# Kernel optimization log

Measured on AMD Instinct MI355X. Metric: run time of the kernel, lower is better.

## Reference

```python
import jax, jax.numpy as jnp
import numpy as np

EPS = 1e-5
K = 20  # n. neighbors


def _lrelu(x):
    return jnp.where(x >= 0, x, 0.2 * x)


def _bn(x, gamma, beta):
    # training-mode batchnorm over all axes except channel axis 1
    axes = tuple(i for i in range(x.ndim) if i != 1)
    m = jnp.mean(x, axis=axes, keepdims=True)
    v = jnp.var(x, axis=axes, keepdims=True)
    shape = [1, x.shape[1]] + [1] * (x.ndim - 2)
    return (x - m) * jax.lax.rsqrt(v + EPS) * gamma.reshape(shape) + beta.reshape(shape)


def _knn(x, k):
    # x: (B, C, N) -> idx (B, N, k) of nearest neighbors (largest negative sq dist)
    xx = jnp.sum(x * x, axis=1)                      # (B, N)
    inner = jnp.einsum('bcn,bcm->bnm', x, x)          # (B, N, N)
    dist = -xx[:, :, None] + 2.0 * inner - xx[:, None, :]
    _, idx = jax.lax.top_k(dist, k)
    return idx


def _graph_feature(x, k):
    # x: (B, C, N) -> edge features (B, 2C, N, k)
    B = x.shape[0]
    idx = _knn(x, k)                                  # (B, N, k)
    xt = jnp.transpose(x, (0, 2, 1))                  # (B, N, C)
    nbr = xt[jnp.arange(B)[:, None, None], idx]       # (B, N, k, C)
    ctr = xt[:, :, None, :]                           # (B, N, 1, C)
    edge = jnp.concatenate([nbr - ctr, jnp.broadcast_to(ctr, nbr.shape)], axis=-1)
    return jnp.transpose(edge, (0, 3, 1, 2))          # (B, 2C, N, k)


def _conv1d(W, x):
    return jnp.einsum('oc,bcn->bon', W, x)


def _conv2d(W, x):
    return jnp.einsum('oc,bcnk->bonk', W, x)


def setup_inputs() -> dict:
    key = jax.random.key(0)
    ks = jax.random.split(key, 10)
    w = lambda k, s: jax.random.normal(k, s, jnp.float32) * 0.05
    d = {
        'x': jax.random.normal(ks[0], (4, 3, 4096), jnp.float32),
        'W1': w(ks[1], (64, 3)),
        'W2': w(ks[2], (64, 128)),
        'W3': w(ks[3], (64, 128)),
        'W4': w(ks[4], (512, 64)),
        'W5': w(ks[5], (512, 704)),
        'W6': w(ks[6], (256, 512)),
        'W7': w(ks[7], (128, 256)),
        'W8': w(ks[8], (2, 128)),
        'bias8': jnp.zeros((2,), jnp.float32),
    }
    bn_ch = [64, 64, 64, 512, 512, 256, 128]
    for i, c in enumerate(bn_ch, start=1):
        d[f'gamma{i}'] = jnp.ones((c,), jnp.float32)
        d[f'beta{i}'] = jnp.zeros((c,), jnp.float32)
    return d


def reference(x, W1, W2, W3, W4, W5, W6, W7, W8, bias8,
              gamma1, beta1, gamma2, beta2, gamma3, beta3, gamma4, beta4,
              gamma5, beta5, gamma6, beta6, gamma7, beta7):
    N = x.shape[2]
    x1 = _lrelu(_bn(_conv1d(W1, x), gamma1, beta1))                 # (B,64,N)
    e2 = _graph_feature(x1, K)                                      # (B,128,N,k)
    x2 = _lrelu(_bn(_conv2d(W2, e2), gamma2, beta2)).max(axis=-1)   # (B,64,N)
    e3 = _graph_feature(x2, K)
    x3 = _lrelu(_bn(_conv2d(W3, e3), gamma3, beta3)).max(axis=-1)   # (B,64,N)
    x6 = _lrelu(_bn(_conv1d(W4, x3), gamma4, beta4))                # (B,512,N)
    x6 = jnp.broadcast_to(x6.max(axis=-1, keepdims=True), (x6.shape[0], x6.shape[1], N))
    x7 = jnp.concatenate([x1, x2, x3, x6], axis=1)                  # (B,704,N)
    x7 = _lrelu(_bn(_conv1d(W5, x7), gamma5, beta5))
    x7 = _lrelu(_bn(_conv1d(W6, x7), gamma6, beta6))
    x7 = _lrelu(_bn(_conv1d(W7, x7), gamma7, beta7))
    return _conv1d(W8, x7) + bias8[None, :, None]                   # (B,2,N)
```

## Files before the change

kernel.cpp:

```cpp
#include <hip/hip_runtime.h>
#include <math.h>

#define NN 4096
#define BB 4
#define NPT (NN*BB)
#define KK 20
#define EPSB 1e-5f

#define AS_STRIDE 132
#define WS_STRIDE 68
#define SKEW(c) ((((((c)>>2)&7))<<2) + (((c)>>5)*28))

__device__ __forceinline__ float lrelu(float x){ return x >= 0.f ? x : 0.2f*x; }

__global__ void conv1_kernel(const float* __restrict__ x, const float* __restrict__ W1,
                             float* __restrict__ xcat){
  __shared__ float Wl[192];
  int tid = threadIdx.x;
  if (tid < 192) Wl[tid] = W1[tid];
  __syncthreads();
  int p = blockIdx.x*4 + (tid >> 6);
  int o = tid & 63;
  int b = p >> 12, n = p & 4095;
  const float* xb = x + (size_t)b*3*NN + n;
  float acc = Wl[o*3+0]*xb[0] + Wl[o*3+1]*xb[NN] + Wl[o*3+2]*xb[2*NN];
  xcat[(size_t)p*192 + o] = acc;
}

__global__ void stats_pm_kernel(const float* __restrict__ buf, int stride, int ofs,
                                float* __restrict__ psum, float* __restrict__ psumsq, int C){
  int tid = threadIdx.x;
  int lane = tid & 63, g = tid >> 6;
  int o = blockIdx.x*64 + lane;
  int p0 = blockIdx.y*256 + g*64;
  float s = 0.f, ss = 0.f;
  for (int i = 0; i < 64; ++i){
    float v = buf[(size_t)(p0+i)*stride + ofs + o];
    s += v; ss += v*v;
  }
  __shared__ float rs[4][64], rss[4][64];
  rs[g][lane] = s; rss[g][lane] = ss;
  __syncthreads();
  if (g == 0){
    s  = rs[0][lane]+rs[1][lane]+rs[2][lane]+rs[3][lane];
    ss = rss[0][lane]+rss[1][lane]+rss[2][lane]+rss[3][lane];
    psum[(size_t)blockIdx.y*C + o] = s;
// ... 12 lines not shown
  for (int i = 0; i < nparts; ++i){
    s  += psum[(size_t)i*C + o];
    ss += psumsq[(size_t)i*C + o];
  }
  float m = s*invcnt;
  float v = ss*invcnt - m*m;
  v = fmaxf(v, 0.f);
  float sc = gamma[o] * rsqrtf(v + EPSB);
  scale[o] = sc;
  shift[o] = beta[o] - m*sc;
}

__global__ void apply_bn_kernel(float* __restrict__ buf, int stride, int ofs, int log2C,
                                const float* __restrict__ scale, const float* __restrict__ shift){
  int i = blockIdx.x*256 + threadIdx.x;
  int o = i & ((1<<log2C)-1);
  int p = i >> log2C;
  size_t a = (size_t)p*stride + ofs + o;
  float e = buf[a]*scale[o] + shift[o];
  buf[a] = lrelu(e);
}

__global__ void xx_kernel(const float* __restrict__ xcat, int stride, int ofs,
                          float* __restrict__ xx){
  int p = blockIdx.x*256 + threadIdx.x;
  const float4* r = (const float4*)(xcat + (size_t)p*stride + ofs);
  float s = 0.f;
  #pragma unroll
  for (int i = 0; i < 16; ++i){ float4 v = r[i]; s += v.x*v.x + v.y*v.y + v.z*v.z + v.w*v.w; }
  xx[p] = s;
}

__global__ void __launch_bounds__(256, 2)
dist_kernel(const float* __restrict__ xcat, int ofs,
            const float* __restrict__ xx, float* __restrict__ dist, int b){
  __shared__ float As[64*AS_STRIDE + 64];
  __shared__ float Bs[64*AS_STRIDE + 64];
  int tid = threadIdx.x;
  int n0 = blockIdx.x*128, m0 = blockIdx.y*128;
  const float* base = xcat + (size_t)b*NN*192 + ofs;
  #pragma unroll
  for (int j = 0; j < 8; ++j){
    int slot = tid + 256*j;
    int row = slot >> 4, c4 = (slot & 15)*4;
    float4 v = *(const float4*)(base + (size_t)(n0+row)*192 + c4);
    As[(c4+0)*AS_STRIDE+SKEW(c4+0)+row]=v.x; As[(c4+1)*AS_STRIDE+SKEW(c4+1)+row]=v.y;
    As[(c4+2)*AS_STRIDE+SKEW(c4+2)+row]=v.z; As[(c4+3)*AS_STRIDE+SKEW(c4+3)+row]=v.w;
    float4 w = *(const float4*)(base + (size_t)(m0+row)*192 + c4);
    Bs[(c4+0)*AS_STRIDE+SKEW(c4+0)+row]=w.x; Bs[(c4+1)*AS_STRIDE+SKEW(c4+1)+row]=w.y;
    Bs[(c4+2)*AS_STRIDE+SKEW(c4+2)+row]=w.z; Bs[(c4+3)*AS_STRIDE+SKEW(c4+3)+row]=w.w;
  }
  __syncthreads();
  int pA = (tid >> 4)*4, oB = (tid & 15)*4;
  float acc[8][8] = {};
  for (int c = 0; c < 64; ++c){
    const float* arow = &As[c*AS_STRIDE + SKEW(c)];
    const float* brow = &Bs[c*AS_STRIDE + SKEW(c)];
    float4 a0 = *(const float4*)&arow[pA];
    float4 a1 = *(const float4*)&arow[pA + 64];
    float4 b0 = *(const float4*)&brow[oB];
    float4 b1 = *(const float4*)&brow[oB + 64];
    float av[8] = {a0.x,a0.y,a0.z,a0.w,a1.x,a1.y,a1.z,a1.w};
    float bv[8] = {b0.x,b0.y,b0.z,b0.w,b1.x,b1.y,b1.z,b1.w};
    #pragma unroll
    for (int i = 0; i < 8; ++i)
      #pragma unroll
      for (int j = 0; j < 8; ++j)
        acc[i][j] += av[i]*bv[j];
  }
  float xm[8];
  #pragma unroll
  for (int j = 0; j < 4; ++j){
    xm[j]   = xx[b*NN + m0 + oB + j];
    xm[4+j] = xx[b*NN + m0 + 64 + oB + j];
  }
  #pragma unroll
  for (int h = 0; h < 2; ++h){
    #pragma unroll
    for (int i = 0; i < 4; ++i){
      int row = n0 + h*64 + pA + i;
      float xn = xx[b*NN + row];
      int ai = h*4 + i;
      float4 w0, w1;
      w0.x = 2.f*acc[ai][0] - xn - xm[0]; w0.y = 2.f*acc[ai][1] - xn - xm[1];
      w0.z = 2.f*acc[ai][2] - xn - xm[2]; w0.w = 2.f*acc[ai][3] - xn - xm[3];
      w1.x = 2.f*acc[ai][4] - xn - xm[4]; w1.y = 2.f*acc[ai][5] - xn - xm[5];
      w1.z = 2.f*acc[ai][6] - xn - xm[6]; w1.w = 2.f*acc[ai][7] - xn - xm[7];
      float* drow = dist + (size_t)row*NN + m0;
      *(float4*)(drow + oB) = w0;
      *(float4*)(drow + 64 + oB) = w1;
    }
  }
}

__global__ void topk_kernel(const float* __restrict__ dist, int* __restrict__ idxout){
  int n = blockIdx.x;
  int tid = threadIdx.x;
  int wv = tid >> 6;
  const float* row = dist + (size_t)n*NN;
  unsigned k[16];
  #pragma unroll
  for (int i = 0; i < 16; ++i){
    unsigned u = __float_as_uint(row[tid + (i<<8)]);
    k[i] = u ^ (unsigned)(((int)u >> 31) | 0x80000000);
  }
  __shared__ unsigned hist[4][256];
  __shared__ unsigned sufx[257];
  __shared__ unsigned selw[1];
  __shared__ unsigned toff[256];
  __shared__ int mred[4];
  unsigned remaining = KK;
  unsigned prefix = 0;
  #pragma unroll
  for (int lvl = 0; lvl < 4; ++lvl){
    int shift = 24 - lvl*8;
    hist[0][tid]=0; hist[1][tid]=0; hist[2][tid]=0; hist[3][tid]=0;
    __syncthreads();
    unsigned pmask = (lvl == 0) ? 0u : (0xFFFFFFFFu << (shift + 8));
    #pragma unroll
    for (int i = 0; i < 16; ++i){
      if ((k[i] & pmask) == prefix)
        atomicAdd(&hist[wv][(k[i] >> shift) & 255], 1u);
    }
    __syncthreads();
    if (tid < 64){
      unsigned h[4];
      #pragma unroll
      for (int q = 0; q < 4; ++q)
        h[q] = hist[0][tid*4+q]+hist[1][tid*4+q]+hist[2][tid*4+q]+hist[3][tid*4+q];
      unsigned lane_sum = h[0]+h[1]+h[2]+h[3];
      unsigned acc = lane_sum;
      #pragma unroll
      for (int s = 1; s < 64; s <<= 1){
        unsigned o = __shfl_down(acc, s);
        if (tid + s < 64) acc += o;
      }
      unsigned excl = acc - lane_sum;
      sufx[tid*4+3] = excl + h[3];
      sufx[tid*4+2] = excl + h[3] + h[2];
      sufx[tid*4+1] = excl + h[3] + h[2] + h[1];
      sufx[tid*4+0] = excl + h[3] + h[2] + h[1] + h[0];
      if (tid == 0) sufx[256] = 0;
    }
    __syncthreads();
    unsigned s_d = sufx[tid], s_d1 = sufx[tid+1];
    if (s_d >= remaining && s_d1 < remaining) selw[0] = tid;
    __syncthreads();
    unsigned d = selw[0];
    remaining -= sufx[d+1];
    prefix |= d << shift;
  }
  unsigned K20 = prefix;
  unsigned r = remaining;
  unsigned mycount = 0;
  #pragma unroll
  for (int i = 0; i < 16; ++i) if (k[i] > K20) mycount++;
  toff[tid] = mycount;
  __syncthreads();
  if (tid < 64){
    unsigned c0=toff[tid*4], c1=toff[tid*4+1], c2=toff[tid*4+2], c3=toff[tid*4+3];
    unsigned lane_sum = c0+c1+c2+c3;
    unsigned acc = lane_sum;
    #pragma unroll
    for (int s = 1; s < 64; s <<= 1){
      unsigned o = __shfl_up(acc, s);
      if ((int)tid - s >= 0) acc += o;
    }
    unsigned excl = acc - lane_sum;
    sufx[tid*4+0] = excl;
    sufx[tid*4+1] = excl + c0;
    sufx[tid*4+2] = excl + c0 + c1;
    sufx[tid*4+3] = excl + c0 + c1 + c2;
  }
  __syncthreads();
  unsigned pos = sufx[tid];
  int* orow = idxout + n*KK;
  #pragma unroll
  for (int i = 0; i < 16; ++i)
    if (k[i] > K20) orow[pos++] = tid + (i<<8);
  unsigned A = KK - r;
  int last = -1;
  for (unsigned t = 0; t < r; ++t){
    int best = 0x7fffffff;
    #pragma unroll
    for (int i = 0; i < 16; ++i){
      int m = tid + (i<<8);
      if (k[i] == K20 && m > last && m < best) best = m;
    }
    #pragma unroll
    for (int s = 32; s > 0; s >>= 1){
      int o = __shfl_down(best, s);
      best = min(best, o);
    }
    if ((tid & 63) == 0) mred[tid >> 6] = best;
    __syncthreads();
    int w = min(min(mred[0],mred[1]), min(mred[2],mred[3]));
    if (tid == 0) orow[A + t] = w;
    last = w;
    __syncthreads();
  }
}

__global__ void ut_kernel(const float* __restrict__ xcat, int ofs, const float* __restrict__ W,
                          float* __restrict__ U, float* __restrict__ T){
  __shared__ float Wl[64*129];
  int tid = threadIdx.x;
  for (int i = tid; i < 64*128; i += 256){
    int o = i >> 7, c = i & 127;
    Wl[o*129 + c] = W[i];
  }
  __syncthreads();
  int g = tid >> 6, lane = tid & 63;
  int p = blockIdx.x*4 + g;
  float xv = xcat[(size_t)p*192 + ofs + lane];
  const float* wr = Wl + lane*129;
  float u = 0.f, t = 0.f;
  for (int c = 0; c < 64; ++c){
    float xc = __shfl(xv, c);
    float wa = wr[c], wb = wr[64+c];
    u += wa*xc;
    t += (wb - wa)*xc;
  }
  U[(size_t)p*64 + lane] = u;
  T[(size_t)p*64 + lane] = t;
}

__global__ void gather_kernel(const float* __restrict__ U, const float* __restrict__ T,
                              const int* __restrict__ idx,
                              float* __restrict__ psum, float* __restrict__ psumsq,
                              float* __restrict__ vmax, float* __restrict__ vmin){
  int tid = threadIdx.x;
  int g = tid >> 6, lane = tid & 63;
  int p0 = blockIdx.x*64 + g*16;
// ... 23 lines not shown
    psumsq[(size_t)blockIdx.x*64 + lane] = ss;
  }
}

__global__ void gapply_kernel(const float* __restrict__ vmax, const float* __restrict__ vmin,
                              const float* __restrict__ scale, const float* __restrict__ shift,
                              float* __restrict__ xcat, int ofs){
  int i = blockIdx.x*256 + threadIdx.x;
  int p = i >> 6, o = i & 63;
  float s = scale[o];
  float v = (s >= 0.f) ? vmax[i] : vmin[i];
  xcat[(size_t)p*192 + ofs + o] = lrelu(s*v + shift[o]);
}

__global__ void __launch_bounds__(256, 2)
mm_kernel(const float* __restrict__ in, int inStride, int inOfs,
          const float* __restrict__ W, int wStride,
          float* __restrict__ out, int outStride,
          const float* __restrict__ bias, int O, int I,
          const float* __restrict__ bnScale, const float* __restrict__ bnShift){
  __shared__ float As[64*AS_STRIDE + 64];
  __shared__ float Ws[64*WS_STRIDE + 64];
  int tid = threadIdx.x;
  int p0 = blockIdx.x*128, o0 = blockIdx.y*64;
  int psub = (tid >> 4)*8, osub = (tid & 15)*4;
  int cgrp = (tid & 15)*4;
  float acc[8][4] = {};
  for (int cc = 0; cc < I; cc += 64){
    float4 sc4 = make_float4(1.f,1.f,1.f,1.f), sh4 = make_float4(0.f,0.f,0.f,0.f);
    if (bnScale){
      sc4 = *(const float4*)(bnScale + cc + cgrp);
      sh4 = *(const float4*)(bnShift + cc + cgrp);
    }
    #pragma unroll
    for (int j = 0; j < 8; ++j){
      int slot = tid + 256*j;
      int row = slot >> 4, c4 = cgrp;
      float4 v = *(const float4*)(in + (size_t)(p0+row)*inStride + inOfs + cc + c4);
      if (bnScale){
        v.x = lrelu(v.x*sc4.x + sh4.x); v.y = lrelu(v.y*sc4.y + sh4.y);
        v.z = lrelu(v.z*sc4.z + sh4.z); v.w = lrelu(v.w*sc4.w + sh4.w);
      }
      As[(c4+0)*AS_STRIDE+SKEW(c4+0)+row]=v.x; As[(c4+1)*AS_STRIDE+SKEW(c4+1)+row]=v.y;
      As[(c4+2)*AS_STRIDE+SKEW(c4+2)+row]=v.z; As[(c4+3)*AS_STRIDE+SKEW(c4+3)+row]=v.w;
    }
    #pragma unroll
    for (int j = 0; j < 4; ++j){
      int slot = tid + 256*j;
      int row = slot >> 4, c4 = cgrp;
      float4 v = *(const float4*)(W + (size_t)(o0+row)*wStride + cc + c4);
      Ws[(c4+0)*WS_STRIDE+SKEW(c4+0)+row]=v.x; Ws[(c4+1)*WS_STRIDE+SKEW(c4+1)+row]=v.y;
      Ws[(c4+2)*WS_STRIDE+SKEW(c4+2)+row]=v.z; Ws[(c4+3)*WS_STRIDE+SKEW(c4+3)+row]=v.w;
    }
    __syncthreads();
    for (int c = 0; c < 64; ++c){
      const float* arow = &As[c*AS_STRIDE + SKEW(c)];
      const float* brow = &Ws[c*WS_STRIDE + SKEW(c)];
      float4 a0 = *(const float4*)&arow[psub];
      float4 a1 = *(const float4*)&arow[psub + 4];
      float4 bb = *(const float4*)&brow[osub];
      float av[8] = {a0.x,a0.y,a0.z,a0.w,a1.x,a1.y,a1.z,a1.w};
      float bv[4] = {bb.x,bb.y,bb.z,bb.w};
      #pragma unroll
      for (int i = 0; i < 8; ++i)
        #pragma unroll
        for (int j = 0; j < 4; ++j)
          acc[i][j] += av[i]*bv[j];
    }
    __syncthreads();
  }
  int bIdx = p0 >> 12;
  float bb0=0.f, bb1=0.f, bb2=0.f, bb3=0.f;
  if (bias){
    bb0 = bias[bIdx*O + o0 + osub + 0];
    bb1 = bias[bIdx*O + o0 + osub + 1];
    bb2 = bias[bIdx*O + o0 + osub + 2];
    bb3 = bias[bIdx*O + o0 + osub + 3];
  }
  #pragma unroll
  for (int i = 0; i < 8; ++i){
    float4 w;
    w.x = acc[i][0]+bb0; w.y = acc[i][1]+bb1; w.z = acc[i][2]+bb2; w.w = acc[i][3]+bb3;
    *(float4*)(out + (size_t)(p0+psub+i)*outStride + o0 + osub) = w;
  }
}

__global__ void __launch_bounds__(256, 2)
mm128_kernel(const float* __restrict__ in, int inStride, int inOfs,
             const float* __restrict__ W, int wStride,
             float* __restrict__ out, int outStride,
             const float* __restrict__ bias, int O, int I,
             const float* __restrict__ bnScale, const float* __restrict__ bnShift){
  __shared__ float As[64*AS_STRIDE + 64];
  __shared__ float Ws[64*AS_STRIDE + 64];
  int tid = threadIdx.x;
  int p0 = blockIdx.x*128, o0 = blockIdx.y*128;
  int pA = (tid >> 4)*4, oB = (tid & 15)*4;
  int cgrp = (tid & 15)*4;
  float acc[8][8] = {};
  for (int cc = 0; cc < I; cc += 64){
    float4 sc4 = make_float4(1.f,1.f,1.f,1.f), sh4 = make_float4(0.f,0.f,0.f,0.f);
    if (bnScale){
      sc4 = *(const float4*)(bnScale + cc + cgrp);
      sh4 = *(const float4*)(bnShift + cc + cgrp);
    }
    #pragma unroll
    for (int j = 0; j < 8; ++j){
      int slot = tid + 256*j;
      int row = slot >> 4, c4 = cgrp;
      float4 v = *(const float4*)(in + (size_t)(p0+row)*inStride + inOfs + cc + c4);
      if (bnScale){
        v.x = lrelu(v.x*sc4.x + sh4.x); v.y = lrelu(v.y*sc4.y + sh4.y);
        v.z = lrelu(v.z*sc4.z + sh4.z); v.w = lrelu(v.w*sc4.w + sh4.w);
      }
      As[(c4+0)*AS_STRIDE+SKEW(c4+0)+row]=v.x; As[(c4+1)*AS_STRIDE+SKEW(c4+1)+row]=v.y;
      As[(c4+2)*AS_STRIDE+SKEW(c4+2)+row]=v.z; As[(c4+3)*AS_STRIDE+SKEW(c4+3)+row]=v.w;
      float4 w = *(const float4*)(W + (size_t)(o0+row)*wStride + cc + c4);
      Ws[(c4+0)*AS_STRIDE+SKEW(c4+0)+row]=w.x; Ws[(c4+1)*AS_STRIDE+SKEW(c4+1)+row]=w.y;
      Ws[(c4+2)*AS_STRIDE+SKEW(c4+2)+row]=w.z; Ws[(c4+3)*AS_STRIDE+SKEW(c4+3)+row]=w.w;
    }
    __syncthreads();
    for (int c = 0; c < 64; ++c){
      const float* arow = &As[c*AS_STRIDE + SKEW(c)];
      const float* brow = &Ws[c*AS_STRIDE + SKEW(c)];
      float4 a0 = *(const float4*)&arow[pA];
      float4 a1 = *(const float4*)&arow[pA + 64];
      float4 b0 = *(const float4*)&brow[oB];
      float4 b1 = *(const float4*)&brow[oB + 64];
      float av[8] = {a0.x,a0.y,a0.z,a0.w,a1.x,a1.y,a1.z,a1.w};
      float bv[8] = {b0.x,b0.y,b0.z,b0.w,b1.x,b1.y,b1.z,b1.w};
      #pragma unroll
      for (int i = 0; i < 8; ++i)
        #pragma unroll
        for (int j = 0; j < 8; ++j)
          acc[i][j] += av[i]*bv[j];
    }
    __syncthreads();
  }
  int bIdx = p0 >> 12;
  float bb[8] = {0.f,0.f,0.f,0.f,0.f,0.f,0.f,0.f};
  if (bias){
    #pragma unroll
    for (int j = 0; j < 4; ++j){
      bb[j]   = bias[bIdx*O + o0 + oB + j];
      bb[4+j] = bias[bIdx*O + o0 + 64 + oB + j];
    }
  }
  #pragma unroll
  for (int h = 0; h < 2; ++h){
    #pragma unroll
    for (int i = 0; i < 4; ++i){
      int row = p0 + h*64 + pA + i;
      int ai = h*4 + i;
      float4 w0, w1;
      w0.x = acc[ai][0]+bb[0]; w0.y = acc[ai][1]+bb[1];
      w0.z = acc[ai][2]+bb[2]; w0.w = acc[ai][3]+bb[3];
      w1.x = acc[ai][4]+bb[4]; w1.y = acc[ai][5]+bb[5];
      w1.z = acc[ai][6]+bb[6]; w1.w = acc[ai][7]+bb[7];
      float* orow = out + (size_t)row*outStride + o0;
      *(float4*)(orow + oB) = w0;
      *(float4*)(orow + 64 + oB) = w1;
    }
  }
}

__global__ void stats4_kernel(const float* __restrict__ r4,
                              float* __restrict__ psum, float* __restrict__ psumsq,
                              float* __restrict__ pmax, float* __restrict__ pmin){
  int tid = threadIdx.x;
  int lane = tid & 63, g = tid >> 6;
  int o = blockIdx.x*64 + lane;
  int p0 = blockIdx.y*256 + g*64;
  float s = 0.f, ss = 0.f, mx = -INFINITY, mn = INFINITY;
  for (int i = 0; i < 64; ++i){
    float v = r4[(size_t)(p0+i)*512 + o];
    s += v; ss += v*v; mx = fmaxf(mx, v); mn = fminf(mn, v);
  }
  __shared__ float rs[4][64], rss[4][64], rmx[4][64], rmn[4][64];
  rs[g][lane]=s; rss[g][lane]=ss; rmx[g][lane]=mx; rmn[g][lane]=mn;
  __syncthreads();
  if (g == 0){
    psum [(size_t)blockIdx.y*512 + o] = rs[0][lane]+rs[1][lane]+rs[2][lane]+rs[3][lane];
    psumsq[(size_t)blockIdx.y*512 + o] = rss[0][lane]+rss[1][lane]+rss[2][lane]+rss[3][lane];
    pmax [(size_t)blockIdx.y*512 + o] = fmaxf(fmaxf(rmx[0][lane],rmx[1][lane]), fmaxf(rmx[2][lane],rmx[3][lane]));
    pmin [(size_t)blockIdx.y*512 + o] = fminf(fminf(rmn[0][lane],rmn[1][lane]), fminf(rmn[2][lane],rmn[3][lane]));
  }
}

__global__ void x6v_kernel(const float* __restrict__ pmax, const float* __restrict__ pmin,
                           const float* __restrict__ scale, const float* __restrict__ shift,
                           float* __restrict__ x6v){
  int t = blockIdx.x*256 + threadIdx.x;
  int b = t >> 9, o = t & 511;
  float mx = -INFINITY, mn = INFINITY;
  for (int pt = b*16; pt < b*16+16; ++pt){
    mx = fmaxf(mx, pmax[(size_t)pt*512 + o]);
    mn = fminf(mn, pmin[(size_t)pt*512 + o]);
  }
  float s = scale[o];
  float v = (s >= 0.f) ? mx : mn;
  x6v[t] = lrelu(s*v + shift[o]);
}

__global__ void bias5_kernel(const float* __restrict__ W5, const float* __restrict__ x6v,
                             float* __restrict__ b5){
  __shared__ float xl[512];
  int tid = threadIdx.x;
  int t = blockIdx.x*256 + tid;
  int b = t >> 9, o = t & 511;
  for (int i = tid; i < 512; i += 256) xl[i] = x6v[(b<<9) + i];
  __syncthreads();
  const float* wr = W5 + (size_t)o*704 + 192;
  float acc = 0.f;
  for (int c = 0; c < 512; ++c) acc += wr[c]*xl[c];
  b5[t] = acc;
}

__global__ void conv8_kernel(const float* __restrict__ r7, const float* __restrict__ W8,
                             const float* __restrict__ bias8,
                             const float* __restrict__ scale, const float* __restrict__ shift,
                             float* __restrict__ out){
  __shared__ float Wl[256];
  __shared__ float scl[128], shl[128];
  int tid = threadIdx.x;
  Wl[tid] = W8[tid];
  if (tid < 128){ scl[tid] = scale[tid]; shl[tid] = shift[tid]; }
  __syncthreads();
  int p = blockIdx.x*256 + tid;
// ... 11 lines not shown
    a1 += v.x*Wl[128+i*4] + v.y*Wl[128+i*4+1] + v.z*Wl[128+i*4+2] + v.w*Wl[128+i*4+3];
  }
  out[(size_t)(b*2+0)*NN + n] = a0 + bias8[0];
  out[(size_t)(b*2+1)*NN + n] = a1 + bias8[1];
}

extern "C" void kernel_launch(void* const* d_in, const int* in_sizes, int n_in,
                              void* d_out, int out_size, void* d_ws, size_t ws_size,
                              hipStream_t stream){
  const float* x     = (const float*)d_in[0];
  const float* W1    = (const float*)d_in[1];
  const float* W2    = (const float*)d_in[2];
  const float* W3    = (const float*)d_in[3];
  const float* W4    = (const float*)d_in[4];
  const float* W5    = (const float*)d_in[5];
  const float* W6    = (const float*)d_in[6];
  const float* W7    = (const float*)d_in[7];
  const float* W8    = (const float*)d_in[8];
  const float* bias8 = (const float*)d_in[9];
  const float* gamma[8]; const float* beta[8];
  for (int i = 1; i <= 7; ++i){
    gamma[i] = (const float*)d_in[10 + 2*(i-1)];
    beta[i]  = (const float*)d_in[11 + 2*(i-1)];
  }
  float* out = (float*)d_out;

  float* ws = (float*)d_ws;
  size_t off = 0;
  float* xcat  = ws + off; off += (size_t)NPT*192;
  float* U     = ws + off; off += (size_t)NPT*64;
  float* T     = ws + off; off += (size_t)NPT*64;
  float* xx    = ws + off; off += NPT;
  int*   idx   = (int*)(ws + off); off += (size_t)NPT*KK;
  float* psum  = ws + off; off += 64*512;
  float* psumsq= ws + off; off += 64*512;
  float* pmax  = ws + off; off += 64*512;
  float* pmin  = ws + off; off += 64*512;
  float* scale = ws + off; off += 512;
  float* shift = ws + off; off += 512;
  float* x6v   = ws + off; off += 2048;
  float* b5    = ws + off; off += 2048;
  float* big   = ws + off;
  float* dist  = big;
  float* vmaxB = big;
  float* vminB = big + (size_t)NPT*64;
  float* r4    = big;
  float* r5    = big;
  float* r6    = big + (size_t)NPT*512;
  float* r7    = big + (size_t)NPT*512 + (size_t)NPT*256;

  conv1_kernel<<<NPT/4, 256, 0, stream>>>(x, W1, xcat);
  stats_pm_kernel<<<dim3(1,64), 256, 0, stream>>>(xcat, 192, 0, psum, psumsq, 64);
  bn_finalize_kernel<<<1, 64, 0, stream>>>(psum, psumsq, 64, gamma[1], beta[1], scale, shift, 1.f/16384.f, 64);
  apply_bn_kernel<<<NPT*64/256, 256, 0, stream>>>(xcat, 192, 0, 6, scale, shift);

  xx_kernel<<<NPT/256, 256, 0, stream>>>(xcat, 192, 0, xx);
  for (int b = 0; b < BB; ++b){
    dist_kernel<<<dim3(32,32), 256, 0, stream>>>(xcat, 0, xx, dist, b);
    topk_kernel<<<NN, 256, 0, stream>>>(dist, idx + (size_t)b*NN*KK);
  }

  ut_kernel<<<NPT/4, 256, 0, stream>>>(xcat, 0, W2, U, T);
  gather_kernel<<<256, 256, 0, stream>>>(U, T, idx, psum, psumsq, vmaxB, vminB);
  bn_finalize_kernel<<<1, 64, 0, stream>>>(psum, psumsq, 256, gamma[2], beta[2], scale, shift, 1.f/327680.f, 64);
  gapply_kernel<<<NPT*64/256, 256, 0, stream>>>(vmaxB, vminB, scale, shift, xcat, 64);

  xx_kernel<<<NPT/256, 256, 0, stream>>>(xcat, 192, 64, xx);
  for (int b = 0; b < BB; ++b){
    dist_kernel<<<dim3(32,32), 256, 0, stream>>>(xcat, 64, xx, dist, b);
    topk_kernel<<<NN, 256, 0, stream>>>(dist, idx + (size_t)b*NN*KK);
  }

  ut_kernel<<<NPT/4, 256, 0, stream>>>(xcat, 64, W3, U, T);
  gather_kernel<<<256, 256, 0, stream>>>(U, T, idx, psum, psumsq, vmaxB, vminB);
  bn_finalize_kernel<<<1, 64, 0, stream>>>(psum, psumsq, 256, gamma[3], beta[3], scale, shift, 1.f/327680.f, 64);
  gapply_kernel<<<NPT*64/256, 256, 0, stream>>>(vmaxB, vminB, scale, shift, xcat, 128);

  mm128_kernel<<<dim3(NPT/128, 4), 256, 0, stream>>>(xcat, 192, 128, W4, 64, r4, 512, nullptr, 512, 64, nullptr, nullptr);
  stats4_kernel<<<dim3(8,64), 256, 0, stream>>>(r4, psum, psumsq, pmax, pmin);
  bn_finalize_kernel<<<1, 512, 0, stream>>>(psum, psumsq, 64, gamma[4], beta[4], scale, shift, 1.f/16384.f, 512);
  x6v_kernel<<<8, 256, 0, stream>>>(pmax, pmin, scale, shift, x6v);
  bias5_kernel<<<8, 256, 0, stream>>>(W5, x6v, b5);

  mm128_kernel<<<dim3(NPT/128, 4), 256, 0, stream>>>(xcat, 192, 0, W5, 704, r5, 512, b5, 512, 192, nullptr, nullptr);
  stats_pm_kernel<<<dim3(8,64), 256, 0, stream>>>(r5, 512, 0, psum, psumsq, 512);
  bn_finalize_kernel<<<1, 512, 0, stream>>>(psum, psumsq, 64, gamma[5], beta[5], scale, shift, 1.f/16384.f, 512);

  mm128_kernel<<<dim3(NPT/128, 2), 256, 0, stream>>>(r5, 512, 0, W6, 512, r6, 256, nullptr, 256, 512, scale, shift);
  stats_pm_kernel<<<dim3(4,64), 256, 0, stream>>>(r6, 256, 0, psum, psumsq, 256);
  bn_finalize_kernel<<<1, 256, 0, stream>>>(psum, psumsq, 64, gamma[6], beta[6], scale, shift, 1.f/16384.f, 256);

  mm_kernel<<<dim3(NPT/128, 2), 256, 0, stream>>>(r6, 256, 0, W7, 256, r7, 128, nullptr, 128, 256, scale, shift);
  stats_pm_kernel<<<dim3(2,64), 256, 0, stream>>>(r7, 128, 0, psum, psumsq, 128);
  bn_finalize_kernel<<<1, 128, 0, stream>>>(psum, psumsq, 64, gamma[7], beta[7], scale, shift, 1.f/16384.f, 128);

  conv8_kernel<<<NPT/256, 256, 0, stream>>>(r7, W8, bias8, scale, shift, out);
}
```

Measured before the change: 1.357 ms.

## Fuse distance matmul with per-thread top-k selection, drop full distance matrix

Replaces the per-batch distance kernel plus radix-select top-k with one fused kernel. It computes distance tiles in shared memory and keeps a running sorted top-20 list per thread over column slices. A small merge kernel then combines the eight partial candidate lists per point. This removes writing and re-reading the 4096x4096 distance matrix for each batch, at the cost of register-heavy insertion sorts and serialized selection work. The matmul kernels also now issue their global loads into registers before the shared-memory stores.

```diff
diff --git a/kernel.cpp b/kernel.cpp
--- a/kernel.cpp
+++ b/kernel.cpp
@@ -12,6 +12,10 @@
 #define SKEW(c) ((((((c)>>2)&7))<<2) + (((c)>>5)*28))
 
 __device__ __forceinline__ float lrelu(float x){ return x >= 0.f ? x : 0.2f*x; }
+
+__device__ __forceinline__ bool kbetter(float v1, int i1, float v2, int i2){
+  return (v1 > v2) || (v1 == v2 && i1 < i2);
+}
 
 __global__ void conv1_kernel(const float* __restrict__ x, const float* __restrict__ W1,
                              float* __restrict__ xcat){
@@ -90,12 +94,14 @@
 }
 
 __global__ void __launch_bounds__(256, 2)
-dist_kernel(const float* __restrict__ xcat, int ofs,
-            const float* __restrict__ xx, float* __restrict__ dist, int b){
+knn_kernel(const float* __restrict__ xcat, int ofs, const float* __restrict__ xx,
+           float* __restrict__ candV, int* __restrict__ candI){
   __shared__ float As[64*AS_STRIDE + 64];
-  __shared__ float Bs[64*AS_STRIDE + 64];
-  int tid = threadIdx.x;
-  int n0 = blockIdx.x*128, m0 = blockIdx.y*128;
+  __shared__ float Bs[64*WS_STRIDE + 64];
+  __shared__ float Sel[64*65];
+  int tid = threadIdx.x;
+  int rt = blockIdx.x, ms = blockIdx.y, b = blockIdx.z;
+  int n0 = rt*128;
   const float* base = xcat + (size_t)b*NN*192 + ofs;
   #pragma unroll
   for (int j = 0; j < 8; ++j){
@@ -104,159 +110,113 @@
     float4 v = *(const float4*)(base + (size_t)(n0+row)*192 + c4);
     As[(c4+0)*AS_STRIDE+SKEW(c4+0)+row]=v.x; As[(c4+1)*AS_STRIDE+SKEW(c4+1)+row]=v.y;
     As[(c4+2)*AS_STRIDE+SKEW(c4+2)+row]=v.z; As[(c4+3)*AS_STRIDE+SKEW(c4+3)+row]=v.w;
-    float4 w = *(const float4*)(base + (size_t)(m0+row)*192 + c4);
-    Bs[(c4+0)*AS_STRIDE+SKEW(c4+0)+row]=w.x; Bs[(c4+1)*AS_STRIDE+SKEW(c4+1)+row]=w.y;
-    Bs[(c4+2)*AS_STRIDE+SKEW(c4+2)+row]=w.z; Bs[(c4+3)*AS_STRIDE+SKEW(c4+3)+row]=w.w;
-  }
-  __syncthreads();
+  }
   int pA = (tid >> 4)*4, oB = (tid & 15)*4;
-  float acc[8][8] = {};
-  for (int c = 0; c < 64; ++c){
-    const float* arow = &As[c*AS_STRIDE + SKEW(c)];
-    const float* brow = &Bs[c*AS_STRIDE + SKEW(c)];
-    float4 a0 = *(const float4*)&arow[pA];
-    float4 a1 = *(const float4*)&arow[pA + 64];
-    float4 b0 = *(const float4*)&brow[oB];
-    float4 b1 = *(const float4*)&brow[oB + 64];
-    float av[8] = {a0.x,a0.y,a0.z,a0.w,a1.x,a1.y,a1.z,a1.w};
-    float bv[8] = {b0.x,b0.y,b0.z,b0.w,b1.x,b1.y,b1.z,b1.w};
-    #pragma unroll
-    for (int i = 0; i < 8; ++i)
+  float xn[8];
+  #pragma unroll
+  for (int i = 0; i < 4; ++i){
+    xn[i]   = xx[b*NN + n0 + pA + i];
+    xn[4+i] = xx[b*NN + n0 + 64 + pA + i];
+  }
+  int srow  = (tid < 128) ? (tid >> 1) : 64 + ((tid - 128) >> 1);
+  int shalf = tid & 1;
+  float tv[20]; int ti[20];
+  #pragma unroll
+  for (int s = 0; s < 20; ++s){ tv[s] = -INFINITY; ti[s] = 0x7fffffff; }
+  for (int ch = 0; ch < 16; ++ch){
+    int m0 = ms*1024 + ch*64;
+    #pragma unroll
+    for (int j = 0; j < 4; ++j){
+      int slot = tid + 256*j;
+      int col = slot >> 4, c4 = (slot & 15)*4;
+      float4 v = *(const float4*)(base + (size_t)(m0+col)*192 + c4);
+      Bs[(c4+0)*WS_STRIDE+SKEW(c4+0)+col]=v.x; Bs[(c4+1)*WS_STRIDE+SKEW(c4+1)+col]=v.y;
+      Bs[(c4+2)*WS_STRIDE+SKEW(c4+2)+col]=v.z; Bs[(c4+3)*WS_STRIDE+SKEW(c4+3)+col]=v.w;
+    }
+    __syncthreads();
+    float acc[8][4] = {};
+    for (int c = 0; c < 64; ++c){
+      const float* arow = &As[c*AS_STRIDE + SKEW(c)];
+      const float* brow = &Bs[c*WS_STRIDE + SKEW(c)];
+      float4 a0 = *(const float4*)&arow[pA];
+      float4 a1 = *(const float4*)&arow[pA + 64];
+      float4 bb = *(const float4*)&brow[oB];
+      float av[8] = {a0.x,a0.y,a0.z,a0.w,a1.x,a1.y,a1.z,a1.w};
+      float bv[4] = {bb.x,bb.y,bb.z,bb.w};
       #pragma unroll
-      for (int j = 0; j < 8; ++j)
-        acc[i][j] += av[i]*bv[j];
-  }
-  float xm[8];
-  #pragma unroll
-  for (int j = 0; j < 4; ++j){
-    xm[j]   = xx[b*NN + m0 + oB + j];
-    xm[4+j] = xx[b*NN + m0 + 64 + oB + j];
-  }
-  #pragma unroll
-  for (int h = 0; h < 2; ++h){
-    #pragma unroll
-    for (int i = 0; i < 4; ++i){
-      int row = n0 + h*64 + pA + i;
-      float xn = xx[b*NN + row];
-      int ai = h*4 + i;
-      float4 w0, w1;
-      w0.x = 2.f*acc[ai][0] - xn - xm[0]; w0.y = 2.f*acc[ai][1] - xn - xm[1];
-      w0.z = 2.f*acc[ai][2] - xn - xm[2]; w0.w = 2.f*acc[ai][3] - xn - xm[3];
-      w1.x = 2.f*acc[ai][4] - xn - xm[4]; w1.y = 2.f*acc[ai][5] - xn - xm[5];
-      w1.z = 2.f*acc[ai][6] - xn - xm[6]; w1.w = 2.f*acc[ai][7] - xn - xm[7];
-      float* drow = dist + (size_t)row*NN + m0;
-      *(float4*)(drow + oB) = w0;
-      *(float4*)(drow + 64 + oB) = w1;
-    }
-  }
-}
-
-__global__ void topk_kernel(const float* __restrict__ dist, int* __restrict__ idxout){
-  int n = blockIdx.x;
-  int tid = threadIdx.x;
-  int wv = tid >> 6;
-  const float* row = dist + (size_t)n*NN;
-  unsigned k[16];
-  #pragma unroll
-  for (int i = 0; i < 16; ++i){
-    unsigned u = __float_as_uint(row[tid + (i<<8)]);
-    k[i] = u ^ (unsigned)(((int)u >> 31) | 0x80000000);
-  }
-  __shared__ unsigned hist[4][256];
-  __shared__ unsigned sufx[257];
-  __shared__ unsigned selw[1];
-  __shared__ unsigned toff[256];
-  __shared__ int mred[4];
-  unsigned remaining = KK;
-  unsigned prefix = 0;
-  #pragma unroll
-  for (int lvl = 0; lvl < 4; ++lvl){
-    int shift = 24 - lvl*8;
-    hist[0][tid]=0; hist[1][tid]=0; hist[2][tid]=0; hist[3][tid]=0;
-    __syncthreads();
-    unsigned pmask = (lvl == 0) ? 0u : (0xFFFFFFFFu << (shift + 8));
-    #pragma unroll
-    for (int i = 0; i < 16; ++i){
-      if ((k[i] & pmask) == prefix)
-        atomicAdd(&hist[wv][(k[i] >> shift) & 255], 1u);
-    }
-    __syncthreads();
-    if (tid < 64){
-      unsigned h[4];
+      for (int i = 0; i < 8; ++i)
+        #pragma unroll
+        for (int j = 0; j < 4; ++j)
+          acc[i][j] += av[i]*bv[j];
+    }
+    float xm[4];
+    #pragma unroll
+    for (int j = 0; j < 4; ++j) xm[j] = xx[b*NN + m0 + oB + j];
+    #pragma unroll
+    for (int h = 0; h < 2; ++h){
       #pragma unroll
-      for (int q = 0; q < 4; ++q)
-        h[q] = hist[0][tid*4+q]+hist[1][tid*4+q]+hist[2][tid*4+q]+hist[3][tid*4+q];
-      unsigned lane_sum = h[0]+h[1]+h[2]+h[3];
-      unsigned acc = lane_sum;
-      #pragma unroll
-      for (int s = 1; s < 64; s <<= 1){
-        unsigned o = __shfl_down(acc, s);
-        if (tid + s < 64) acc += o;
+      for (int i = 0; i < 4; ++i){
+        int ai = h*4 + i;
+        float4 w;
+        w.x = 2.f*acc[ai][0] - xn[ai] - xm[0];
+        w.y = 2.f*acc[ai][1] - xn[ai] - xm[1];
+        w.z = 2.f*acc[ai][2] - xn[ai] - xm[2];
+        w.w = 2.f*acc[ai][3] - xn[ai] - xm[3];
+        *(float4*)&Sel[(pA+i)*65 + oB] = w;
       }
-      unsigned excl = acc - lane_sum;
-      sufx[tid*4+3] = excl + h[3];
-      sufx[tid*4+2] = excl + h[3] + h[2];
-      sufx[tid*4+1] = excl + h[3] + h[2] + h[1];
-      sufx[tid*4+0] = excl + h[3] + h[2] + h[1] + h[0];
-      if (tid == 0) sufx[256] = 0;
-    }
-    __syncthreads();
-    unsigned s_d = sufx[tid], s_d1 = sufx[tid+1];
-    if (s_d >= remaining && s_d1 < remaining) selw[0] = tid;
-    __syncthreads();
-    unsigned d = selw[0];
-    remaining -= sufx[d+1];
-    prefix |= d << shift;
-  }
-  unsigned K20 = prefix;
-  unsigned r = remaining;
-  unsigned mycount = 0;
-  #pragma unroll
-  for (int i = 0; i < 16; ++i) if (k[i] > K20) mycount++;
-  toff[tid] = mycount;
-  __syncthreads();
-  if (tid < 64){
-    unsigned c0=toff[tid*4], c1=toff[tid*4+1], c2=toff[tid*4+2], c3=toff[tid*4+3];
-    unsigned lane_sum = c0+c1+c2+c3;
-    unsigned acc = lane_sum;
-    #pragma unroll
-    for (int s = 1; s < 64; s <<= 1){
-      unsigned o = __shfl_up(acc, s);
-      if ((int)tid - s >= 0) acc += o;
-    }
-    unsigned excl = acc - lane_sum;
-    sufx[tid*4+0] = excl;
-    sufx[tid*4+1] = excl + c0;
-    sufx[tid*4+2] = excl + c0 + c1;
-    sufx[tid*4+3] = excl + c0 + c1 + c2;
-  }
-  __syncthreads();
-  unsigned pos = sufx[tid];
-  int* orow = idxout + n*KK;
-  #pragma unroll
-  for (int i = 0; i < 16; ++i)
-    if (k[i] > K20) orow[pos++] = tid + (i<<8);
-  unsigned A = KK - r;
-  int last = -1;
-  for (unsigned t = 0; t < r; ++t){
-    int best = 0x7fffffff;
-    #pragma unroll
-    for (int i = 0; i < 16; ++i){
-      int m = tid + (i<<8);
-      if (k[i] == K20 && m > last && m < best) best = m;
-    }
-    #pragma unroll
-    for (int s = 32; s > 0; s >>= 1){
-      int o = __shfl_down(best, s);
-      best = min(best, o);
-    }
-    if ((tid & 63) == 0) mred[tid >> 6] = best;
-    __syncthreads();
-    int w = min(min(mred[0],mred[1]), min(mred[2],mred[3]));
-    if (tid == 0) orow[A + t] = w;
-    last = w;
-    __syncthreads();
-  }
+      __syncthreads();
+      if ((h == 0) == (tid < 128)){
+        int lrow = srow - h*64;
+        const float* sp = &Sel[lrow*65 + shalf*32];
+        int mbase = m0 + shalf*32;
+        for (int i2 = 0; i2 < 32; ++i2){
+          float v = sp[i2]; int id = mbase + i2;
+          if (kbetter(v, id, tv[19], ti[19])){
+            float cv = v; int ci = id;
+            #pragma unroll
+            for (int s = 0; s < 20; ++s){
+              bool takes = kbetter(cv, ci, tv[s], ti[s]);
+              float nv = takes ? cv : tv[s]; int ni = takes ? ci : ti[s];
+              cv = takes ? tv[s] : cv;       ci = takes ? ti[s] : ci;
+              tv[s] = nv; ti[s] = ni;
+            }
+          }
+        }
+      }
+      __syncthreads();
+    }
+  }
+  size_t o = ((size_t)((b*4 + ms)*2 + shalf)*NN + n0 + srow)*KK;
+  #pragma unroll
+  for (int s = 0; s < 20; ++s){ candV[o+s] = tv[s]; candI[o+s] = ti[s]; }
+}
+
+__global__ void knnmerge_kernel(const float* __restrict__ candV, const int* __restrict__ candI,
+                                int* __restrict__ idxout){
+  int r = blockIdx.x*256 + threadIdx.x;
+  int b = r >> 12, n = r & 4095;
+  float tv[20]; int ti[20];
+  #pragma unroll
+  for (int s = 0; s < 20; ++s){ tv[s] = -INFINITY; ti[s] = 0x7fffffff; }
+  for (int q = 0; q < 8; ++q){
+    size_t o = ((size_t)(b*8 + q)*NN + n)*KK;
+    for (int k = 0; k < KK; ++k){
+      float v = candV[o+k]; int id = candI[o+k];
+      if (kbetter(v, id, tv[19], ti[19])){
+        float cv = v; int ci = id;
+        #pragma unroll
+        for (int s = 0; s < 20; ++s){
+          bool takes = kbetter(cv, ci, tv[s], ti[s]);
+          float nv = takes ? cv : tv[s]; int ni = takes ? ci : ti[s];
+          cv = takes ? tv[s] : cv;       ci = takes ? ti[s] : ci;
+          tv[s] = nv; ti[s] = ni;
+        }
+      }
+    }
+  }
+  int* orow = idxout + (size_t)r*KK;
+  #pragma unroll
+  for (int s = 0; s < 20; ++s) orow[s] = ti[s];
 }
 
 __global__ void ut_kernel(const float* __restrict__ xcat, int ofs, const float* __restrict__ W,
@@ -346,11 +306,21 @@
       sc4 = *(const float4*)(bnScale + cc + cgrp);
       sh4 = *(const float4*)(bnShift + cc + cgrp);
     }
+    float4 vin[8], vw[4];
     #pragma unroll
     for (int j = 0; j < 8; ++j){
-      int slot = tid + 256*j;
-      int row = slot >> 4, c4 = cgrp;
-      float4 v = *(const float4*)(in + (size_t)(p0+row)*inStride + inOfs + cc + c4);
+      int row = (tid + 256*j) >> 4;
+      vin[j] = *(const float4*)(in + (size_t)(p0+row)*inStride + inOfs + cc + cgrp);
+    }
+    #pragma unroll
+    for (int j = 0; j < 4; ++j){
+      int row = (tid + 256*j) >> 4;
+      vw[j] = *(const float4*)(W + (size_t)(o0+row)*wStride + cc + cgrp);
+    }
+    #pragma unroll
+    for (int j = 0; j < 8; ++j){
+      int row = (tid + 256*j) >> 4, c4 = cgrp;
+      float4 v = vin[j];
       if (bnScale){
         v.x = lrelu(v.x*sc4.x + sh4.x); v.y = lrelu(v.y*sc4.y + sh4.y);
         v.z = lrelu(v.z*sc4.z + sh4.z); v.w = lrelu(v.w*sc4.w + sh4.w);
@@ -360,9 +330,8 @@
     }
     #pragma unroll
     for (int j = 0; j < 4; ++j){
-      int slot = tid + 256*j;
-      int row = slot >> 4, c4 = cgrp;
-      float4 v = *(const float4*)(W + (size_t)(o0+row)*wStride + cc + c4);
+      int row = (tid + 256*j) >> 4, c4 = cgrp;
+      float4 v = vw[j];
       Ws[(c4+0)*WS_STRIDE+SKEW(c4+0)+row]=v.x; Ws[(c4+1)*WS_STRIDE+SKEW(c4+1)+row]=v.y;
       Ws[(c4+2)*WS_STRIDE+SKEW(c4+2)+row]=v.z; Ws[(c4+3)*WS_STRIDE+SKEW(c4+3)+row]=v.w;
     }
@@ -418,18 +387,24 @@
       sc4 = *(const float4*)(bnScale + cc + cgrp);
       sh4 = *(const float4*)(bnShift + cc + cgrp);
     }
+    float4 vin[8], vw[8];
     #pragma unroll
     for (int j = 0; j < 8; ++j){
-      int slot = tid + 256*j;
-      int row = slot >> 4, c4 = cgrp;
-      float4 v = *(const float4*)(in + (size_t)(p0+row)*inStride + inOfs + cc + c4);
+      int row = (tid + 256*j) >> 4;
+      vin[j] = *(const float4*)(in + (size_t)(p0+row)*inStride + inOfs + cc + cgrp);
+      vw[j]  = *(const float4*)(W + (size_t)(o0+row)*wStride + cc + cgrp);
+    }
+    #pragma unroll
+    for (int j = 0; j < 8; ++j){
+      int row = (tid + 256*j) >> 4, c4 = cgrp;
+      float4 v = vin[j];
       if (bnScale){
         v.x = lrelu(v.x*sc4.x + sh4.x); v.y = lrelu(v.y*sc4.y + sh4.y);
         v.z = lrelu(v.z*sc4.z + sh4.z); v.w = lrelu(v.w*sc4.w + sh4.w);
       }
       As[(c4+0)*AS_STRIDE+SKEW(c4+0)+row]=v.x; As[(c4+1)*AS_STRIDE+SKEW(c4+1)+row]=v.y;
       As[(c4+2)*AS_STRIDE+SKEW(c4+2)+row]=v.z; As[(c4+3)*AS_STRIDE+SKEW(c4+3)+row]=v.w;
-      float4 w = *(const float4*)(W + (size_t)(o0+row)*wStride + cc + c4);
+      float4 w = vw[j];
       Ws[(c4+0)*AS_STRIDE+SKEW(c4+0)+row]=w.x; Ws[(c4+1)*AS_STRIDE+SKEW(c4+1)+row]=w.y;
       Ws[(c4+2)*AS_STRIDE+SKEW(c4+2)+row]=w.z; Ws[(c4+3)*AS_STRIDE+SKEW(c4+3)+row]=w.w;
     }
@@ -594,7 +569,8 @@
   float* x6v   = ws + off; off += 2048;
   float* b5    = ws + off; off += 2048;
   float* big   = ws + off;
-  float* dist  = big;
+  float* candV = big;
+  int*   candI = (int*)(big + (size_t)32*NN*KK);
   float* vmaxB = big;
   float* vminB = big + (size_t)NPT*64;
   float* r4    = big;
@@ -608,10 +584,8 @@
   apply_bn_kernel<<<NPT*64/256, 256, 0, stream>>>(xcat, 192, 0, 6, scale, shift);
 
   xx_kernel<<<NPT/256, 256, 0, stream>>>(xcat, 192, 0, xx);
-  for (int b = 0; b < BB; ++b){
-    dist_kernel<<<dim3(32,32), 256, 0, stream>>>(xcat, 0, xx, dist, b);
-    topk_kernel<<<NN, 256, 0, stream>>>(dist, idx + (size_t)b*NN*KK);
-  }
+  knn_kernel<<<dim3(32,4,BB), 256, 0, stream>>>(xcat, 0, xx, candV, candI);
+  knnmerge_kernel<<<NPT/256, 256, 0, stream>>>(candV, candI, idx);
 
   ut_kernel<<<NPT/4, 256, 0, stream>>>(xcat, 0, W2, U, T);
   gather_kernel<<<256, 256, 0, stream>>>(U, T, idx, psum, psumsq, vmaxB, vminB);
@@ -619,10 +593,8 @@
   gapply_kernel<<<NPT*64/256, 256, 0, stream>>>(vmaxB, vminB, scale, shift, xcat, 64);
 
   xx_kernel<<<NPT/256, 256, 0, stream>>>(xcat, 192, 64, xx);
-  for (int b = 0; b < BB; ++b){
-    dist_kernel<<<dim3(32,32), 256, 0, stream>>>(xcat, 64, xx, dist, b);
-    topk_kernel<<<NN, 256, 0, stream>>>(dist, idx + (size_t)b*NN*KK);
-  }
+  knn_kernel<<<dim3(32,4,BB), 256, 0, stream>>>(xcat, 64, xx, candV, candI);
+  knnmerge_kernel<<<NPT/256, 256, 0, stream>>>(candV, candI, idx);
 
   ut_kernel<<<NPT/4, 256, 0, stream>>>(xcat, 64, W3, U, T);
   gather_kernel<<<256, 256, 0, stream>>>(U, T, idx, psum, psumsq, vmaxB, vminB);
```

Result: slower. 2.700 ms (+98.9%).

## Fuse conv4 GEMM with BN stats/max-min reduction and batch tile global loads

Applied to the files above, without the earlier changes.

Replaces the separate conv4 matmul plus stats4 pass with one kernel that computes the GEMM tile and reduces sum, sum of squares, max and min per channel in registers and shared memory. This avoids writing and re-reading the 16384x512 intermediate. Per-block partials double to 128 slots, so bn_finalize and x6v now reduce over more partials. Separately, the dist and mm kernels issue all global float4 loads into registers before the shared-memory stores to raise memory-level parallelism, at the cost of more registers.

```diff
diff --git a/kernel.cpp b/kernel.cpp
--- a/kernel.cpp
+++ b/kernel.cpp
@@ -97,14 +97,21 @@
   int tid = threadIdx.x;
   int n0 = blockIdx.x*128, m0 = blockIdx.y*128;
   const float* base = xcat + (size_t)b*NN*192 + ofs;
+  int cgrp = (tid & 15)*4;
+  float4 vin[8], vw[8];
   #pragma unroll
   for (int j = 0; j < 8; ++j){
-    int slot = tid + 256*j;
-    int row = slot >> 4, c4 = (slot & 15)*4;
-    float4 v = *(const float4*)(base + (size_t)(n0+row)*192 + c4);
+    int row = (tid + 256*j) >> 4;
+    vin[j] = *(const float4*)(base + (size_t)(n0+row)*192 + cgrp);
+    vw[j]  = *(const float4*)(base + (size_t)(m0+row)*192 + cgrp);
+  }
+  #pragma unroll
+  for (int j = 0; j < 8; ++j){
+    int row = (tid + 256*j) >> 4, c4 = cgrp;
+    float4 v = vin[j];
     As[(c4+0)*AS_STRIDE+SKEW(c4+0)+row]=v.x; As[(c4+1)*AS_STRIDE+SKEW(c4+1)+row]=v.y;
     As[(c4+2)*AS_STRIDE+SKEW(c4+2)+row]=v.z; As[(c4+3)*AS_STRIDE+SKEW(c4+3)+row]=v.w;
-    float4 w = *(const float4*)(base + (size_t)(m0+row)*192 + c4);
+    float4 w = vw[j];
     Bs[(c4+0)*AS_STRIDE+SKEW(c4+0)+row]=w.x; Bs[(c4+1)*AS_STRIDE+SKEW(c4+1)+row]=w.y;
     Bs[(c4+2)*AS_STRIDE+SKEW(c4+2)+row]=w.z; Bs[(c4+3)*AS_STRIDE+SKEW(c4+3)+row]=w.w;
   }
@@ -346,11 +353,21 @@
       sc4 = *(const float4*)(bnScale + cc + cgrp);
       sh4 = *(const float4*)(bnShift + cc + cgrp);
     }
+    float4 vin[8], vw[4];
     #pragma unroll
     for (int j = 0; j < 8; ++j){
-      int slot = tid + 256*j;
-      int row = slot >> 4, c4 = cgrp;
-      float4 v = *(const float4*)(in + (size_t)(p0+row)*inStride + inOfs + cc + c4);
+      int row = (tid + 256*j) >> 4;
+      vin[j] = *(const float4*)(in + (size_t)(p0+row)*inStride + inOfs + cc + cgrp);
+    }
+    #pragma unroll
+    for (int j = 0; j < 4; ++j){
+      int row = (tid + 256*j) >> 4;
+      vw[j] = *(const float4*)(W + (size_t)(o0+row)*wStride + cc + cgrp);
+    }
+    #pragma unroll
+    for (int j = 0; j < 8; ++j){
+      int row = (tid + 256*j) >> 4, c4 = cgrp;
+      float4 v = vin[j];
       if (bnScale){
         v.x = lrelu(v.x*sc4.x + sh4.x); v.y = lrelu(v.y*sc4.y + sh4.y);
         v.z = lrelu(v.z*sc4.z + sh4.z); v.w = lrelu(v.w*sc4.w + sh4.w);
@@ -360,9 +377,8 @@
     }
     #pragma unroll
     for (int j = 0; j < 4; ++j){
-      int slot = tid + 256*j;
-      int row = slot >> 4, c4 = cgrp;
-      float4 v = *(const float4*)(W + (size_t)(o0+row)*wStride + cc + c4);
+      int row = (tid + 256*j) >> 4, c4 = cgrp;
+      float4 v = vw[j];
       Ws[(c4+0)*WS_STRIDE+SKEW(c4+0)+row]=v.x; Ws[(c4+1)*WS_STRIDE+SKEW(c4+1)+row]=v.y;
       Ws[(c4+2)*WS_STRIDE+SKEW(c4+2)+row]=v.z; Ws[(c4+3)*WS_STRIDE+SKEW(c4+3)+row]=v.w;
     }
@@ -418,18 +434,24 @@
       sc4 = *(const float4*)(bnScale + cc + cgrp);
       sh4 = *(const float4*)(bnShift + cc + cgrp);
     }
+    float4 vin[8], vw[8];
     #pragma unroll
     for (int j = 0; j < 8; ++j){
-      int slot = tid + 256*j;
-      int row = slot >> 4, c4 = cgrp;
-      float4 v = *(const float4*)(in + (size_t)(p0+row)*inStride + inOfs + cc + c4);
+      int row = (tid + 256*j) >> 4;
+      vin[j] = *(const float4*)(in + (size_t)(p0+row)*inStride + inOfs + cc + cgrp);
+      vw[j]  = *(const float4*)(W + (size_t)(o0+row)*wStride + cc + cgrp);
+    }
+    #pragma unroll
+    for (int j = 0; j < 8; ++j){
+      int row = (tid + 256*j) >> 4, c4 = cgrp;
+      float4 v = vin[j];
       if (bnScale){
         v.x = lrelu(v.x*sc4.x + sh4.x); v.y = lrelu(v.y*sc4.y + sh4.y);
         v.z = lrelu(v.z*sc4.z + sh4.z); v.w = lrelu(v.w*sc4.w + sh4.w);
       }
       As[(c4+0)*AS_STRIDE+SKEW(c4+0)+row]=v.x; As[(c4+1)*AS_STRIDE+SKEW(c4+1)+row]=v.y;
       As[(c4+2)*AS_STRIDE+SKEW(c4+2)+row]=v.z; As[(c4+3)*AS_STRIDE+SKEW(c4+3)+row]=v.w;
-      float4 w = *(const float4*)(W + (size_t)(o0+row)*wStride + cc + c4);
+      float4 w = vw[j];
       Ws[(c4+0)*AS_STRIDE+SKEW(c4+0)+row]=w.x; Ws[(c4+1)*AS_STRIDE+SKEW(c4+1)+row]=w.y;
       Ws[(c4+2)*AS_STRIDE+SKEW(c4+2)+row]=w.z; Ws[(c4+3)*AS_STRIDE+SKEW(c4+3)+row]=w.w;
     }
@@ -478,26 +500,82 @@
   }
 }
 
-__global__ void stats4_kernel(const float* __restrict__ r4,
-                              float* __restrict__ psum, float* __restrict__ psumsq,
-                              float* __restrict__ pmax, float* __restrict__ pmin){
-  int tid = threadIdx.x;
-  int lane = tid & 63, g = tid >> 6;
-  int o = blockIdx.x*64 + lane;
-  int p0 = blockIdx.y*256 + g*64;
-  float s = 0.f, ss = 0.f, mx = -INFINITY, mn = INFINITY;
-  for (int i = 0; i < 64; ++i){
-    float v = r4[(size_t)(p0+i)*512 + o];
-    s += v; ss += v*v; mx = fmaxf(mx, v); mn = fminf(mn, v);
-  }
-  __shared__ float rs[4][64], rss[4][64], rmx[4][64], rmn[4][64];
-  rs[g][lane]=s; rss[g][lane]=ss; rmx[g][lane]=mx; rmn[g][lane]=mn;
-  __syncthreads();
-  if (g == 0){
-    psum [(size_t)blockIdx.y*512 + o] = rs[0][lane]+rs[1][lane]+rs[2][lane]+rs[3][lane];
-    psumsq[(size_t)blockIdx.y*512 + o] = rss[0][lane]+rss[1][lane]+rss[2][lane]+rss[3][lane];
-    pmax [(size_t)blockIdx.y*512 + o] = fmaxf(fmaxf(rmx[0][lane],rmx[1][lane]), fmaxf(rmx[2][lane],rmx[3][lane]));
-    pmin [(size_t)blockIdx.y*512 + o] = fminf(fminf(rmn[0][lane],rmn[1][lane]), fminf(rmn[2][lane],rmn[3][lane]));
+__global__ void __launch_bounds__(256, 2)
+conv4stats_kernel(const float* __restrict__ xcat, const float* __restrict__ W4,
+                  float* __restrict__ psum, float* __restrict__ psumsq,
+                  float* __restrict__ pmax, float* __restrict__ pmin){
+  __shared__ float As[64*AS_STRIDE + 64];
+  __shared__ float Ws[64*AS_STRIDE + 64];
+  int tid = threadIdx.x;
+  int p0 = blockIdx.x*128, o0 = blockIdx.y*128;
+  int pA = (tid >> 4)*4, oB = (tid & 15)*4;
+  int cgrp = (tid & 15)*4;
+  float4 vin[8], vw[8];
+  #pragma unroll
+  for (int j = 0; j < 8; ++j){
+    int row = (tid + 256*j) >> 4;
+    vin[j] = *(const float4*)(xcat + (size_t)(p0+row)*192 + 128 + cgrp);
+    vw[j]  = *(const float4*)(W4 + (size_t)(o0+row)*64 + cgrp);
+  }
+  #pragma unroll
+  for (int j = 0; j < 8; ++j){
+    int row = (tid + 256*j) >> 4, c4 = cgrp;
+    float4 v = vin[j];
+    As[(c4+0)*AS_STRIDE+SKEW(c4+0)+row]=v.x; As[(c4+1)*AS_STRIDE+SKEW(c4+1)+row]=v.y;
+    As[(c4+2)*AS_STRIDE+SKEW(c4+2)+row]=v.z; As[(c4+3)*AS_STRIDE+SKEW(c4+3)+row]=v.w;
+    float4 w = vw[j];
+    Ws[(c4+0)*AS_STRIDE+SKEW(c4+0)+row]=w.x; Ws[(c4+1)*AS_STRIDE+SKEW(c4+1)+row]=w.y;
+    Ws[(c4+2)*AS_STRIDE+SKEW(c4+2)+row]=w.z; Ws[(c4+3)*AS_STRIDE+SKEW(c4+3)+row]=w.w;
+  }
+  __syncthreads();
+  float acc[8][8] = {};
+  for (int c = 0; c < 64; ++c){
+    const float* arow = &As[c*AS_STRIDE + SKEW(c)];
+    const float* brow = &Ws[c*AS_STRIDE + SKEW(c)];
+    float4 a0 = *(const float4*)&arow[pA];
+    float4 a1 = *(const float4*)&arow[pA + 64];
+    float4 b0 = *(const float4*)&brow[oB];
+    float4 b1 = *(const float4*)&brow[oB + 64];
+    float av[8] = {a0.x,a0.y,a0.z,a0.w,a1.x,a1.y,a1.z,a1.w};
+    float bv[8] = {b0.x,b0.y,b0.z,b0.w,b1.x,b1.y,b1.z,b1.w};
+    #pragma unroll
+    for (int i = 0; i < 8; ++i)
+      #pragma unroll
+      for (int j = 0; j < 8; ++j)
+        acc[i][j] += av[i]*bv[j];
+  }
+  float cs[8], cq[8], cmx[8], cmn[8];
+  #pragma unroll
+  for (int j = 0; j < 8; ++j){
+    float s = 0.f, q = 0.f, mx = -INFINITY, mn = INFINITY;
+    #pragma unroll
+    for (int i = 0; i < 8; ++i){
+      float v = acc[i][j];
+      s += v; q += v*v; mx = fmaxf(mx, v); mn = fminf(mn, v);
+    }
+    cs[j]=s; cq[j]=q; cmx[j]=mx; cmn[j]=mn;
+  }
+  __syncthreads();
+  int r = tid >> 4;
+  #pragma unroll
+  for (int j = 0; j < 8; ++j){
+    int col = (j < 4) ? (oB + j) : (64 + oB + (j-4));
+    As[r*128 + col]        = cs[j];
+    As[2048 + r*128 + col] = cq[j];
+    Ws[r*128 + col]        = cmx[j];
+    Ws[2048 + r*128 + col] = cmn[j];
+  }
+  __syncthreads();
+  if (tid < 128){
+    float ts = 0.f, tq = 0.f, tm = -INFINITY, tn = INFINITY;
+    for (int rr = 0; rr < 16; ++rr){
+      ts += As[rr*128 + tid];
+      tq += As[2048 + rr*128 + tid];
+      tm = fmaxf(tm, Ws[rr*128 + tid]);
+      tn = fminf(tn, Ws[2048 + rr*128 + tid]);
+    }
+    size_t slot = (size_t)blockIdx.x*512 + o0 + tid;
+    psum[slot] = ts; psumsq[slot] = tq; pmax[slot] = tm; pmin[slot] = tn;
   }
 }
 
@@ -507,7 +585,7 @@
   int t = blockIdx.x*256 + threadIdx.x;
   int b = t >> 9, o = t & 511;
   float mx = -INFINITY, mn = INFINITY;
-  for (int pt = b*16; pt < b*16+16; ++pt){
+  for (int pt = b*32; pt < b*32+32; ++pt){
     mx = fmaxf(mx, pmax[(size_t)pt*512 + o]);
     mn = fminf(mn, pmin[(size_t)pt*512 + o]);
   }
@@ -585,10 +663,10 @@
   float* T     = ws + off; off += (size_t)NPT*64;
   float* xx    = ws + off; off += NPT;
   int*   idx   = (int*)(ws + off); off += (size_t)NPT*KK;
-  float* psum  = ws + off; off += 64*512;
-  float* psumsq= ws + off; off += 64*512;
-  float* pmax  = ws + off; off += 64*512;
-  float* pmin  = ws + off; off += 64*512;
+  float* psum  = ws + off; off += 128*512;
+  float* psumsq= ws + off; off += 128*512;
+  float* pmax  = ws + off; off += 128*512;
+  float* pmin  = ws + off; off += 128*512;
   float* scale = ws + off; off += 512;
   float* shift = ws + off; off += 512;
   float* x6v   = ws + off; off += 2048;
@@ -597,7 +675,6 @@
   float* dist  = big;
   float* vmaxB = big;
   float* vminB = big + (size_t)NPT*64;
-  float* r4    = big;
   float* r5    = big;
   float* r6    = big + (size_t)NPT*512;
   float* r7    = big + (size_t)NPT*512 + (size_t)NPT*256;
@@ -629,9 +706,8 @@
   bn_finalize_kernel<<<1, 64, 0, stream>>>(psum, psumsq, 256, gamma[3], beta[3], scale, shift, 1.f/327680.f, 64);
   gapply_kernel<<<NPT*64/256, 256, 0, stream>>>(vmaxB, vminB, scale, shift, xcat, 128);
 
-  mm128_kernel<<<dim3(NPT/128, 4), 256, 0, stream>>>(xcat, 192, 128, W4, 64, r4, 512, nullptr, 512, 64, nullptr, nullptr);
-  stats4_kernel<<<dim3(8,64), 256, 0, stream>>>(r4, psum, psumsq, pmax, pmin);
-  bn_finalize_kernel<<<1, 512, 0, stream>>>(psum, psumsq, 64, gamma[4], beta[4], scale, shift, 1.f/16384.f, 512);
+  conv4stats_kernel<<<dim3(NPT/128, 4), 256, 0, stream>>>(xcat, W4, psum, psumsq, pmax, pmin);
+  bn_finalize_kernel<<<1, 512, 0, stream>>>(psum, psumsq, 128, gamma[4], beta[4], scale, shift, 1.f/16384.f, 512);
   x6v_kernel<<<8, 256, 0, stream>>>(pmax, pmin, scale, shift, x6v);
   bias5_kernel<<<8, 256, 0, stream>>>(W5, x6v, b5);
 
```

New measurement: 1.356 ms. About the same (-0.1%).
